# Optimization experiments

Hardware: AMD Instinct MI355X
Metric: run time of the kernel (lower is better)

The kernel has to match this reference:

```python
import jax, jax.numpy as jnp
import numpy as np

A, D, F = 2048, 64, 12  # atoms, depth, filter_length


def _chemconv(x, conn, bond, filters):
    # x: (A, D); conn: (A, A, F); bond: (A, F, 2); filters: (D, F, D+2)
    # node_connection = conn.transpose(1,2) @ x -> (A, F, D)
    ncon = jnp.einsum('anf,nd->afd', conn, x)
    combined = jnp.concatenate([ncon, bond], axis=2)  # (A, F, D+2)
    # broadcast-multiply by filters then sum over last two dims -> (A, out_depth)
    return jnp.einsum('afc,ofc->ao', combined, filters)


def setup_inputs() -> dict:
    key = jax.random.key(0)
    k1, k2, k3, k4, k5 = jax.random.split(key, 5)
    x = jax.random.normal(k1, (A, D), dtype=jnp.float32)
    conn = jax.random.uniform(k2, (A, A, F), dtype=jnp.float32)
    bond = jax.random.normal(k3, (A, F, 2), dtype=jnp.float32)
    scale = 1.0 / D  # filters.data.normal_() * (1/in_depth)
    f0 = jax.random.normal(k4, (D, F, D + 2), dtype=jnp.float32) * scale
    f1 = jax.random.normal(k5, (D, F, D + 2), dtype=jnp.float32) * scale
    return {
        'node_property_tensor': x,
        'connectivity_tensor': conn,
        'bond_property_tensor': bond,
        'filters0': f0,
        'filters1': f1,
    }


def reference(node_property_tensor, connectivity_tensor, bond_property_tensor, filters0, filters1):
    x = node_property_tensor
    out = x
    for filt in (filters0, filters1):
        # each ChemConv layer is applied twice (same weights), per the torch code
        out = jax.nn.relu(_chemconv(out, connectivity_tensor, bond_property_tensor, filt))
        out = _chemconv(out, connectivity_tensor, bond_property_tensor, filt)
        out = out + x  # residual to the original block input
        out = jax.nn.relu(out)
    return out
```

## Files before the change

kernel.cpp:

```cpp
#include <hip/hip_runtime.h>


#define A_N 2048
#define D_N 64
#define F_N 12
#define K_TOTAL (A_N * F_N)
#define NSPLIT 16
#define KSEG (K_TOTAL / NSPLIT)
#define BK 64
#define LDB 72

typedef short short8 __attribute__((ext_vector_type(8)));
typedef float f32x4 __attribute__((ext_vector_type(4)));

__device__ __forceinline__ unsigned pk_bf16(float a, float b) {
  unsigned ua = __float_as_uint(a);
  unsigned ub = __float_as_uint(b);
  ua += 0x7fffu + ((ua >> 16) & 1u);
  ub += 0x7fffu + ((ub >> 16) & 1u);
  return (ua >> 16) | (ub & 0xffff0000u);
}

__global__ void k_transpose_x(const float* __restrict__ x, float* __restrict__ xt) {
  __shared__ float ld[64][65];
  int m0 = blockIdx.x * 64;
  int t = threadIdx.x;
  int r = t >> 2, cq = (t & 3) * 16;
  const float4* src = (const float4*)(x + (size_t)(m0 + r) * 64 + cq);
#pragma unroll
  for (int i = 0; i < 4; ++i) {
    float4 v = src[i];
    ld[r][cq + i * 4 + 0] = v.x;
    ld[r][cq + i * 4 + 1] = v.y;
    ld[r][cq + i * 4 + 2] = v.z;
    ld[r][cq + i * 4 + 3] = v.w;
  }
  __syncthreads();
  int c = t >> 2, ml0 = (t & 3) * 16;
  float4* dst = (float4*)(xt + (size_t)c * 2048 + m0 + ml0);
#pragma unroll
  for (int i = 0; i < 4; ++i) {
    float4 v;
    v.x = ld[ml0 + i * 4 + 0][c];
    v.y = ld[ml0 + i * 4 + 1][c];
    v.z = ld[ml0 + i * 4 + 2][c];
    v.w = ld[ml0 + i * 4 + 3][c];
    dst[i] = v;
  }
}

__global__ void k_bterm(const float* __restrict__ bond, const float* __restrict__ f0,
                        const float* __restrict__ f1, float* __restrict__ bt0,
                        float* __restrict__ bt1) {
  int a = blockIdx.x * 64 + (threadIdx.x & 63);
  int o = blockIdx.y * 4 + (threadIdx.x >> 6);
  float s0 = 0.f, s1 = 0.f;
#pragma unroll
  for (int f = 0; f < F_N; ++f) {
#pragma unroll
    for (int j = 0; j < 2; ++j) {
      float bv = bond[a * 24 + f * 2 + j];
      s0 += bv * f0[o * 792 + f * 66 + 64 + j];
      s1 += bv * f1[o * 792 + f * 66 + 64 + j];
    }
  }
  bt0[o * 2048 + a] = s0;
  bt1[o * 2048 + a] = s1;
}

__global__ void k_g(const float* __restrict__ vt, const float* __restrict__ filt,
                    unsigned* __restrict__ gt ) {
  __shared__ float W[12][64];
  int o = blockIdx.y;
  int t = threadIdx.x;
  for (int i = t; i < 768; i += 256) W[i >> 6][i & 63] = filt[o * 792 + (i >> 6) * 66 + (i & 63)];
  __syncthreads();
  int n = blockIdx.x * 256 + t;
  float acc[12] = {0.f, 0.f, 0.f, 0.f, 0.f, 0.f, 0.f, 0.f, 0.f, 0.f, 0.f, 0.f};
#pragma unroll 4
  for (int d = 0; d < 64; ++d) {
    float v = vt[d * 2048 + n];
#pragma unroll
    for (int f = 0; f < F_N; ++f) acc[f] += v * W[f][d];
  }
  unsigned* dst = gt + ((size_t)o * K_TOTAL + n * 12) / 2;
#pragma unroll
  for (int i = 0; i < 6; ++i) dst[i] = pk_bf16(acc[2 * i], acc[2 * i + 1]);
}

__launch_bounds__(256, 2)
__global__ void k_big(const float* __restrict__ conn, const unsigned short* __restrict__ gt,
                      float* __restrict__ part) {
  __shared__ unsigned short smem[2 * 64 * LDB];
  unsigned short* As = smem;
  unsigned short* Bs = smem + 64 * LDB;

  int mt = blockIdx.x;
  int ks = blockIdx.y;
  int r0 = mt * 64;
  int k0 = ks * KSEG;
  int t = threadIdx.x, lane = t & 63, wave = t >> 6;
  int o0 = (wave & 1) * 32, n0 = (wave >> 1) * 32;

  f32x4 zero = {0.f, 0.f, 0.f, 0.f};
  f32x4 acc[2][2];
  acc[0][0] = zero; acc[0][1] = zero; acc[1][0] = zero; acc[1][1] = zero;

  int srow = t >> 2, scq = (t & 3) * 16;
  const float* connp = conn + (size_t)(r0 + srow) * K_TOTAL + k0 + scq;
  const unsigned short* gtp = gt + (size_t)srow * K_TOTAL + k0 + scq;
  unsigned short* bsw = Bs + srow * LDB + scq;
  unsigned short* asw = As + srow * LDB + scq;

  int arow = (lane & 15) * LDB + ((lane >> 4) << 3);

  for (int kb = 0; kb < KSEG / BK; ++kb) {
    float4 c0 = *(const float4*)(connp + 0);
    float4 c1 = *(const float4*)(connp + 4);
    float4 c2 = *(const float4*)(connp + 8);
    float4 c3 = *(const float4*)(connp + 12);
    uint4 g0 = *(const uint4*)(gtp);
    uint4 g1 = *((const uint4*)(gtp) + 1);
    __syncthreads();
    uint4 wb0, wb1;
    wb0.x = pk_bf16(c0.x, c0.y); wb0.y = pk_bf16(c0.z, c0.w);
    wb0.z = pk_bf16(c1.x, c1.y); wb0.w = pk_bf16(c1.z, c1.w);
    wb1.x = pk_bf16(c2.x, c2.y); wb1.y = pk_bf16(c2.z, c2.w);
    wb1.z = pk_bf16(c3.x, c3.y); wb1.w = pk_bf16(c3.z, c3.w);
    *(uint4*)(bsw) = wb0;
    *(uint4*)(bsw + 8) = wb1;
    *(uint4*)(asw) = g0;
    *(uint4*)(asw + 8) = g1;
    __syncthreads();
#pragma unroll
    for (int kk = 0; kk < 2; ++kk) {
      int kof = kk * 32 + arow;
      short8 a0 = *(const short8*)(As + o0 * LDB + kof);
      short8 a1 = *(const short8*)(As + (o0 + 16) * LDB + kof);
      short8 b0 = *(const short8*)(Bs + n0 * LDB + kof);
      short8 b1 = *(const short8*)(Bs + (n0 + 16) * LDB + kof);
      acc[0][0] = __builtin_amdgcn_mfma_f32_16x16x32_bf16(a0, b0, acc[0][0], 0, 0, 0);
      acc[0][1] = __builtin_amdgcn_mfma_f32_16x16x32_bf16(a0, b1, acc[0][1], 0, 0, 0);
      acc[1][0] = __builtin_amdgcn_mfma_f32_16x16x32_bf16(a1, b0, acc[1][0], 0, 0, 0);
      acc[1][1] = __builtin_amdgcn_mfma_f32_16x16x32_bf16(a1, b1, acc[1][1], 0, 0, 0);
    }
    connp += BK;
    gtp += BK;
  }

  float* pp = part + (size_t)ks * (64 * 2048);
  int quad = (lane >> 4) << 2;
  int mcol = lane & 15;
#pragma unroll
  for (int i = 0; i < 2; ++i) {
#pragma unroll
    for (int j = 0; j < 2; ++j) {
#pragma unroll
      for (int r = 0; r < 4; ++r) {
        int o = o0 + i * 16 + quad + r;
        int m = r0 + n0 + j * 16 + mcol;
        pp[o * 2048 + m] = acc[i][j][r];
      }
    }
  }
}

__global__ void k_reduce(const float* __restrict__ part, const float* __restrict__ bt,
                         const float* __restrict__ xt, float* __restrict__ curt,
                         float* __restrict__ outp, int residual, int final_layer) {
  int idx = blockIdx.x * 256 + threadIdx.x;
  float s = bt[idx];
#pragma unroll
  for (int sI = 0; sI < NSPLIT; ++sI) s += part[(size_t)sI * (64 * 2048) + idx];
  if (residual) s += xt[idx];
  s = fmaxf(s, 0.f);
  curt[idx] = s;
  if (final_layer) {
    int o = idx >> 11, m = idx & 2047;
    outp[m * 64 + o] = s;
  }
}

extern "C" void kernel_launch(void* const* d_in, const int* in_sizes, int n_in,
                              void* d_out, int out_size, void* d_ws, size_t ws_size,
                              hipStream_t stream) {
  const float* x    = (const float*)d_in[0];
  const float* conn = (const float*)d_in[1];
  const float* bond = (const float*)d_in[2];
  const float* f0   = (const float*)d_in[3];
  const float* f1   = (const float*)d_in[4];
  float* out = (float*)d_out;

  char* ws = (char*)d_ws;
  float* xt   = (float*)(ws + 0);
  float* curt = (float*)(ws + 524288);
  float* bt0  = (float*)(ws + 1048576);
  float* bt1  = (float*)(ws + 1572864);
  unsigned short* gt = (unsigned short*)(ws + 2097152);
  float* part = (float*)(ws + 5242880);

  k_transpose_x<<<32, 256, 0, stream>>>(x, xt);
  k_bterm<<<dim3(32, 16), 256, 0, stream>>>(bond, f0, f1, bt0, bt1);

  for (int layer = 0; layer < 4; ++layer) {
    const float* filt = (layer < 2) ? f0 : f1;
    const float* bt   = (layer < 2) ? bt0 : bt1;
    const float* vin  = (layer == 0) ? xt : curt;
    k_g<<<dim3(8, 64), 256, 0, stream>>>(vin, filt, (unsigned*)gt);
    k_big<<<dim3(32, NSPLIT), 256, 0, stream>>>(conn, gt, part);
    k_reduce<<<512, 256, 0, stream>>>(part, bt, xt, curt, out, layer & 1, layer == 3);
  }
}
```

Baseline: 487.9 us.

## Pre-convert connectivity to bf16 once and use LDS-free 32x32 MFMA waves

Adds a one-time kernel that converts the fp32 connectivity tensor to bf16 in workspace. The four big GEMM passes then read half as many bytes and skip the per-layer conversion. The GEMM kernel drops shared memory and barriers: each wave loads operands straight from global memory into 32x32x16 bf16 MFMAs, with the split-K factor raised to 32. The cost is an extra full read and write of the conn tensor up front, reduced operand reuse across waves, and twice as many partial sums for the reduction to add.

```diff
diff --git a/kernel.cpp b/kernel.cpp
--- a/kernel.cpp
+++ b/kernel.cpp
@@ -5,13 +5,12 @@
 #define D_N 64
 #define F_N 12
 #define K_TOTAL (A_N * F_N)
-#define NSPLIT 16
+#define NSPLIT 32
 #define KSEG (K_TOTAL / NSPLIT)
-#define BK 64
-#define LDB 72
+#define KSTEPS (KSEG / 16)
 
 typedef short short8 __attribute__((ext_vector_type(8)));
-typedef float f32x4 __attribute__((ext_vector_type(4)));
+typedef float f32x16 __attribute__((ext_vector_type(16)));
 
 __device__ __forceinline__ unsigned pk_bf16(float a, float b) {
   unsigned ua = __float_as_uint(a);
@@ -19,6 +18,19 @@
   ua += 0x7fffu + ((ua >> 16) & 1u);
   ub += 0x7fffu + ((ub >> 16) & 1u);
   return (ua >> 16) | (ub & 0xffff0000u);
+}
+
+__global__ void k_conv(const float* __restrict__ conn, uint4* __restrict__ connb) {
+  size_t i = (size_t)blockIdx.x * 256 + threadIdx.x;
+  const float4* src = (const float4*)conn + i * 2;
+  float4 c0 = src[0];
+  float4 c1 = src[1];
+  uint4 o;
+  o.x = pk_bf16(c0.x, c0.y);
+  o.y = pk_bf16(c0.z, c0.w);
+  o.z = pk_bf16(c1.x, c1.y);
+  o.w = pk_bf16(c1.z, c1.w);
+  connb[i] = o;
 }
 
 __global__ void k_transpose_x(const float* __restrict__ x, float* __restrict__ xt) {
@@ -88,80 +100,40 @@
   for (int i = 0; i < 6; ++i) dst[i] = pk_bf16(acc[2 * i], acc[2 * i + 1]);
 }
 
-__launch_bounds__(256, 2)
-__global__ void k_big(const float* __restrict__ conn, const unsigned short* __restrict__ gt,
-                      float* __restrict__ part) {
-  __shared__ unsigned short smem[2 * 64 * LDB];
-  unsigned short* As = smem;
-  unsigned short* Bs = smem + 64 * LDB;
+__launch_bounds__(256)
+__global__ void k_big(const unsigned short* __restrict__ connb,
+                      const unsigned short* __restrict__ gt, float* __restrict__ part) {
+  int t = threadIdx.x, lane = t & 63;
+  int w = blockIdx.x * 4 + (t >> 6);
+  int mt = w >> 6;
+  int r = w & 63;
+  int ks = r >> 1;
+  int ot = r & 1;
+  int m0 = mt * 32, o0 = ot * 32, k0 = ks * KSEG;
 
-  int mt = blockIdx.x;
-  int ks = blockIdx.y;
-  int r0 = mt * 64;
-  int k0 = ks * KSEG;
-  int t = threadIdx.x, lane = t & 63, wave = t >> 6;
-  int o0 = (wave & 1) * 32, n0 = (wave >> 1) * 32;
+  const short8* ap = (const short8*)(gt + (size_t)(o0 + (lane & 31)) * K_TOTAL + k0 + ((lane >> 5) << 3));
+  const short8* bp = (const short8*)(connb + (size_t)(m0 + (lane & 31)) * K_TOTAL + k0 + ((lane >> 5) << 3));
 
-  f32x4 zero = {0.f, 0.f, 0.f, 0.f};
-  f32x4 acc[2][2];
-  acc[0][0] = zero; acc[0][1] = zero; acc[1][0] = zero; acc[1][1] = zero;
+  f32x16 acc;
+#pragma unroll
+  for (int i = 0; i < 16; ++i) acc[i] = 0.f;
 
-  int srow = t >> 2, scq = (t & 3) * 16;
-  const float* connp = conn + (size_t)(r0 + srow) * K_TOTAL + k0 + scq;
-  const unsigned short* gtp = gt + (size_t)srow * K_TOTAL + k0 + scq;
-  unsigned short* bsw = Bs + srow * LDB + scq;
-  unsigned short* asw = As + srow * LDB + scq;
-
-  int arow = (lane & 15) * LDB + ((lane >> 4) << 3);
-
-  for (int kb = 0; kb < KSEG / BK; ++kb) {
-    float4 c0 = *(const float4*)(connp + 0);
-    float4 c1 = *(const float4*)(connp + 4);
-    float4 c2 = *(const float4*)(connp + 8);
-    float4 c3 = *(const float4*)(connp + 12);
-    uint4 g0 = *(const uint4*)(gtp);
-    uint4 g1 = *((const uint4*)(gtp) + 1);
-    __syncthreads();
-    uint4 wb0, wb1;
-    wb0.x = pk_bf16(c0.x, c0.y); wb0.y = pk_bf16(c0.z, c0.w);
-    wb0.z = pk_bf16(c1.x, c1.y); wb0.w = pk_bf16(c1.z, c1.w);
-    wb1.x = pk_bf16(c2.x, c2.y); wb1.y = pk_bf16(c2.z, c2.w);
-    wb1.z = pk_bf16(c3.x, c3.y); wb1.w = pk_bf16(c3.z, c3.w);
-    *(uint4*)(bsw) = wb0;
-    *(uint4*)(bsw + 8) = wb1;
-    *(uint4*)(asw) = g0;
-    *(uint4*)(asw + 8) = g1;
-    __syncthreads();
-#pragma unroll
-    for (int kk = 0; kk < 2; ++kk) {
-      int kof = kk * 32 + arow;
-      short8 a0 = *(const short8*)(As + o0 * LDB + kof);
-      short8 a1 = *(const short8*)(As + (o0 + 16) * LDB + kof);
-      short8 b0 = *(const short8*)(Bs + n0 * LDB + kof);
-      short8 b1 = *(const short8*)(Bs + (n0 + 16) * LDB + kof);
-      acc[0][0] = __builtin_amdgcn_mfma_f32_16x16x32_bf16(a0, b0, acc[0][0], 0, 0, 0);
-      acc[0][1] = __builtin_amdgcn_mfma_f32_16x16x32_bf16(a0, b1, acc[0][1], 0, 0, 0);
-      acc[1][0] = __builtin_amdgcn_mfma_f32_16x16x32_bf16(a1, b0, acc[1][0], 0, 0, 0);
-      acc[1][1] = __builtin_amdgcn_mfma_f32_16x16x32_bf16(a1, b1, acc[1][1], 0, 0, 0);
-    }
-    connp += BK;
-    gtp += BK;
+#pragma unroll 4
+  for (int k = 0; k < KSTEPS; ++k) {
+    short8 a = ap[0];
+    short8 b = bp[0];
+    acc = __builtin_amdgcn_mfma_f32_32x32x16_bf16(a, b, acc, 0, 0, 0);
+    ap += 2;
+    bp += 2;
   }
 
   float* pp = part + (size_t)ks * (64 * 2048);
-  int quad = (lane >> 4) << 2;
-  int mcol = lane & 15;
+  int m = m0 + (lane & 31);
+  int rbase = o0 + 4 * (lane >> 5);
 #pragma unroll
-  for (int i = 0; i < 2; ++i) {
-#pragma unroll
-    for (int j = 0; j < 2; ++j) {
-#pragma unroll
-      for (int r = 0; r < 4; ++r) {
-        int o = o0 + i * 16 + quad + r;
-        int m = r0 + n0 + j * 16 + mcol;
-        pp[o * 2048 + m] = acc[i][j][r];
-      }
-    }
+  for (int rg = 0; rg < 16; ++rg) {
+    int o = rbase + (rg & 3) + 8 * (rg >> 2);
+    pp[o * 2048 + m] = acc[rg];
   }
 }
 
@@ -198,7 +170,9 @@
   float* bt1  = (float*)(ws + 1572864);
   unsigned short* gt = (unsigned short*)(ws + 2097152);
   float* part = (float*)(ws + 5242880);
+  unsigned short* connb = (unsigned short*)(ws + 33554432);
 
+  k_conv<<<24576, 256, 0, stream>>>(conn, (uint4*)connb);
   k_transpose_x<<<32, 256, 0, stream>>>(x, xt);
   k_bterm<<<dim3(32, 16), 256, 0, stream>>>(bond, f0, f1, bt0, bt1);
 
@@ -207,7 +181,7 @@
     const float* bt   = (layer < 2) ? bt0 : bt1;
     const float* vin  = (layer == 0) ? xt : curt;
     k_g<<<dim3(8, 64), 256, 0, stream>>>(vin, filt, (unsigned*)gt);
-    k_big<<<dim3(32, NSPLIT), 256, 0, stream>>>(conn, gt, part);
+    k_big<<<1024, 256, 0, stream>>>(connb, gt, part);
     k_reduce<<<512, 256, 0, stream>>>(part, bt, xt, curt, out, layer & 1, layer == 3);
   }
 }
```

Result: slower. 600.5 us (+23.1%).
